# Performance work log

Measured on AMD Instinct MI355X. Metric: run time of the kernel, lower is better.

## Reference

```python
import jax, jax.numpy as jnp
import numpy as np
import math

CUTOFF = 6.0
NUM_RADIAL = 96
HID = 128
NUM_GRAPHS = 4
NODES_PER_GRAPH = 4000
BOX = 67.0
EPS = 1e-10


def _layernorm(x):
    m = jnp.mean(x, axis=-1, keepdims=True)
    v = jnp.var(x, axis=-1, keepdims=True)
    return (x - m) / jnp.sqrt(v + 1e-5)


def _rbf(dist):
    # rbf_emb: exp-scaled gaussians with cosine cutoff envelope
    start = math.exp(-CUTOFF)
    means = jnp.linspace(start, 1.0, NUM_RADIAL).astype(dist.dtype)
    beta = (2.0 / NUM_RADIAL * (1.0 - start)) ** -2
    d = dist[:, None]
    env = 0.5 * (jnp.cos(d * jnp.pi / CUTOFF) + 1.0) * (d < CUTOFF).astype(dist.dtype)
    return env * jnp.exp(-beta * jnp.square(jnp.exp(-d) - means))


def _forward(pos, rl_w1, rl_b1, rl_w2, rl_b2, ne_w, ne_b, sv_w, sv_b,
             l3_w1, l3_b1, l3_w2, l3_b2, mp_ln_w, mp_ln_b,
             xp_w1, xp_b1, xp_w2, xp_b2, rp_w, rp_b,
             ip_w1, ip_b1, ip_w2, ip_b2,
             fte_eq_w, fte_w1, fte_b1, fte_w2, fte_b2,
             out_w, out_b, z, batch, edge_index):
    N = pos.shape[0]
    silu = jax.nn.silu
    j, i = edge_index[0], edge_index[1]

    vecs = pos[j] - pos[i]                       # [E,3]
    dist = jnp.linalg.norm(vecs, axis=-1)        # [E]
    r_emb = _rbf(dist)                           # [E,R]
    r_hid = silu(r_emb @ rl_w1 + rl_b1) @ rl_w2 + rl_b2
    rbounds = 0.5 * (jnp.cos(dist * jnp.pi / CUTOFF) + 1.0)
    r_hid = rbounds[:, None] * r_hid             # [E,H]

    # NeighborEmb: s = ln(lin(onehot(z))) + scatter_add_i(ln(lin(onehot(z)))[j] * r_hid)
    z1h = jax.nn.one_hot(z, 95, dtype=pos.dtype)
    h0 = _layernorm(z1h @ ne_w + ne_b)           # [N,H]
    s = h0 + jax.ops.segment_sum(h0[j] * r_hid, i, num_segments=N)

    vec = jnp.zeros((N, 3, HID), pos.dtype)

    ed = vecs / (dist[:, None] + EPS)            # edge_diff [E,3]
    ec = jnp.cross(pos[i], pos[j])
    ec = ec / (jnp.linalg.norm(ec, axis=1, keepdims=True) + EPS)
    ev = jnp.cross(ed, ec)
    frame = jnp.stack([ed, ec, ev], axis=-1)     # [E,3(space),3(frame)]

    # S_vector: scatter_add_i( s_lin[j] outer edge_diff * r_hid )
    s_lin = silu(s @ sv_w + sv_b)
    msg = s_lin[j][:, None, :] * (r_hid[:, None, :] * ed[:, :, None])  # [E,3,H]
    S = jax.ops.segment_sum(msg, i, num_segments=N)                    # [N,3,H]

    def scalarize(Se):
        sc = jnp.einsum('edh,edf->efh', Se, frame)                     # [E,3,H]
        sc = sc.at[:, 1, :].set(jnp.abs(sc[:, 1, :]))
        p = jnp.transpose(sc, (0, 2, 1))                               # [E,H,3]
        out = silu(p @ l3_w1 + l3_b1) @ l3_w2 + l3_b2                  # [E,H,1]
        return (out + p[:, :, :1])[..., 0]                             # [E,H]

    scalar3 = scalarize(S[i])
    scalar4 = scalarize(S[j])
    ew = jnp.concatenate([scalar3, scalar4], axis=-1) * rbounds[:, None]
    ew = jnp.concatenate([ew, r_hid, r_emb], axis=-1)                  # [E,3H+R]

    # EquiMessagePassing (only one layer executes: source loops range(1))
    xln = _layernorm(s) * mp_ln_w + mp_ln_b
    xh = silu(xln @ xp_w1 + xp_b1) @ xp_w2 + xp_b2                     # [N,3H]
    rbfh = (r_emb @ rp_w + rp_b) * (silu(ew @ ip_w1 + ip_b1) @ ip_w2 + ip_b2)
    m = xh[j] * rbfh                                                   # [E,3H]
    m1, m2, m3 = jnp.split(m, 3, axis=-1)
    m2 = m2 / jnp.sqrt(3.0)
    vmsg = (vec[j] * m2[:, None, :] + m3[:, None, :] * ed[:, :, None]) / jnp.sqrt(float(HID))
    s = s + jax.ops.segment_sum(m1, i, num_segments=N)
    vec = vec + jax.ops.segment_sum(vmsg, i, num_segments=N)

    # FTE (node_frame == 0 in LEFTNet-Z: use invariant norm channel)
    vp = jnp.einsum('ndh,hk->ndk', vec, fte_eq_w)                      # [N,3,2H]
    v1, v2 = jnp.split(vp, 2, axis=-1)
    scalar = jnp.sqrt(jnp.sum(v1 * v1, axis=1) + EPS)                  # [N,H]
    vec_dot = jnp.sum(v1 * v2, axis=1) / jnp.sqrt(float(HID))
    xh2 = silu(jnp.concatenate([s, scalar], axis=-1) @ fte_w1 + fte_b1) @ fte_w2 + fte_b2
    a1, a2, a3 = jnp.split(xh2, 3, axis=-1)
    s = s + (a1 + a2 * vec_dot) / jnp.sqrt(2.0)
    vec = vec + a3[:, None, :] * v2

    out = s @ out_w + out_b                                            # [N,T]
    num = jax.ops.segment_sum(out, batch, num_segments=NUM_GRAPHS)
    cnt = jax.ops.segment_sum(jnp.ones((N,), out.dtype), batch, num_segments=NUM_GRAPHS)
    out = num / cnt[:, None]                                           # mean readout
    return out  # y_std=1, y_mean=0


def _lin_init(key, fi, fo, bias=True):
    k1, k2 = jax.random.split(key)
    lim = 1.0 / np.sqrt(fi)
    w = jax.random.uniform(k1, (fi, fo), jnp.float32, -lim, lim)
    if not bias:
        return w
    b = jax.random.uniform(k2, (fo,), jnp.float32, -lim, lim)
    return w, b


def setup_inputs() -> dict:
    rng = np.random.default_rng(0)
    N = NUM_GRAPHS * NODES_PER_GRAPH
    pos_np = (rng.random((N, 3)) * BOX).astype(np.float32)
    batch_np = np.repeat(np.arange(NUM_GRAPHS), NODES_PER_GRAPH).astype(np.int64)
    z_np = rng.integers(0, 95, size=(N,)).astype(np.int64)
    rows, cols = [], []
    for g in range(NUM_GRAPHS):
        p = pos_np[g * NODES_PER_GRAPH:(g + 1) * NODES_PER_GRAPH]
        d2 = ((p[:, None, :] - p[None, :, :]) ** 2).sum(-1)
        a, b = np.nonzero((d2 < CUTOFF ** 2) & (d2 > 0.0))
        rows.append(a + g * NODES_PER_GRAPH)
        cols.append(b + g * NODES_PER_GRAPH)
    edge_index = np.stack([np.concatenate(rows), np.concatenate(cols)]).astype(np.int64)

    keys = jax.random.split(jax.random.key(0), 16)
    rl_w1, rl_b1 = _lin_init(keys[0], NUM_RADIAL, HID)
    rl_w2, rl_b2 = _lin_init(keys[1], HID, HID)
    ne_w, ne_b = _lin_init(keys[2], 95, HID)
    sv_w, sv_b = _lin_init(keys[3], HID, HID)
    l3_w1, l3_b1 = _lin_init(keys[4], 3, HID // 4)
    l3_w2, l3_b2 = _lin_init(keys[5], HID // 4, 1)
    xp_w1, xp_b1 = _lin_init(keys[6], HID, HID)
    xp_w2, xp_b2 = _lin_init(keys[7], HID, 3 * HID)
    rp_w, rp_b = _lin_init(keys[8], NUM_RADIAL, 3 * HID)
    ip_w1, ip_b1 = _lin_init(keys[9], 3 * HID + NUM_RADIAL, 3 * HID)
    ip_w2, ip_b2 = _lin_init(keys[10], 3 * HID, 3 * HID)
    fte_eq_w = _lin_init(keys[11], HID, 2 * HID, bias=False)
    fte_w1, fte_b1 = _lin_init(keys[12], 2 * HID, HID)
    fte_w2, fte_b2 = _lin_init(keys[13], HID, 3 * HID)
    out_w, out_b = _lin_init(keys[14], HID, 1)

    return {
        'pos': jnp.asarray(pos_np), 'z': jnp.asarray(z_np),
        'batch': jnp.asarray(batch_np), 'edge_index': jnp.asarray(edge_index),
        'rl_w1': rl_w1, 'rl_b1': rl_b1, 'rl_w2': rl_w2, 'rl_b2': rl_b2,
        'ne_w': ne_w, 'ne_b': ne_b, 'sv_w': sv_w, 'sv_b': sv_b,
        'l3_w1': l3_w1, 'l3_b1': l3_b1, 'l3_w2': l3_w2, 'l3_b2': l3_b2,
        'mp_ln_w': jnp.ones((HID,), jnp.float32), 'mp_ln_b': jnp.zeros((HID,), jnp.float32),
        'xp_w1': xp_w1, 'xp_b1': xp_b1, 'xp_w2': xp_w2, 'xp_b2': xp_b2,
        'rp_w': rp_w, 'rp_b': rp_b,
        'ip_w1': ip_w1, 'ip_b1': ip_b1, 'ip_w2': ip_w2, 'ip_b2': ip_b2,
        'fte_eq_w': fte_eq_w, 'fte_w1': fte_w1, 'fte_b1': fte_b1,
        'fte_w2': fte_w2, 'fte_b2': fte_b2, 'out_w': out_w, 'out_b': out_b,
    }


def reference(pos, rl_w1, rl_b1, rl_w2, rl_b2, ne_w, ne_b, sv_w, sv_b,
              l3_w1, l3_b1, l3_w2, l3_b2, mp_ln_w, mp_ln_b,
              xp_w1, xp_b1, xp_w2, xp_b2, rp_w, rp_b,
              ip_w1, ip_b1, ip_w2, ip_b2,
              fte_eq_w, fte_w1, fte_b1, fte_w2, fte_b2,
              out_w, out_b, z, batch, edge_index):
    return _forward(pos, rl_w1, rl_b1, rl_w2, rl_b2, ne_w, ne_b, sv_w, sv_b,
                    l3_w1, l3_b1, l3_w2, l3_b2, mp_ln_w, mp_ln_b,
                    xp_w1, xp_b1, xp_w2, xp_b2, rp_w, rp_b,
                    ip_w1, ip_b1, ip_w2, ip_b2,
                    fte_eq_w, fte_w1, fte_b1, fte_w2, fte_b2,
                    out_w, out_b, z, batch, edge_index)
```

## Files before the change

kernel.cpp:

```cpp
#include <hip/hip_runtime.h>
#include <hip/hip_bf16.h>
#include <math.h>

#define NRAD 96
#define HIDDIM 128
typedef unsigned short ushortT;

typedef __attribute__((ext_vector_type(8))) short bf8_t;
typedef __attribute__((ext_vector_type(4))) float f4_t;

#if defined(__has_builtin)
#  if __has_builtin(__builtin_amdgcn_global_load_lds)
#    define HAVE_GLDS 1
#  endif
#  if __has_builtin(__builtin_amdgcn_rcpf)
#    define RCPF(x) __builtin_amdgcn_rcpf(x)
#  endif
#  if __has_builtin(__builtin_amdgcn_exp2f)
#    define EXP2F(x) __builtin_amdgcn_exp2f(x)
#  endif
#  if __has_builtin(__builtin_amdgcn_cosf)
#    define COSR(x) __builtin_amdgcn_cosf(x)
#  endif
#endif
#ifndef RCPF
#  define RCPF(x) (1.f/(x))
#endif
#ifndef EXP2F
#  define EXP2F(x) exp2f(x)
#endif
#ifndef COSR
#  define COSR(x) cosf(6.2831853071795864f*(x))
#endif
#define LOG2E 1.44269504088896f
#define LN2   0.69314718055995f

__device__ __forceinline__ float silu_f(float x){
  return x * RCPF(1.f + EXP2F(-LOG2E*x));
}
__device__ __forceinline__ float b2f(ushortT u){ return __uint_as_float(((unsigned int)u) << 16); }
__device__ __forceinline__ ushortT f2b(float x){
  unsigned int u = __float_as_uint(x);
  unsigned int r = (u + 0x7fffu + ((u >> 16) & 1u)) >> 16;
  return (ushortT)r;
}

#ifdef HAVE_GLDS
__device__ __forceinline__ void glds16(const ushortT* g, ushortT* l){
  __builtin_amdgcn_global_load_lds(
      (const __attribute__((address_space(1))) ushortT*)g,
      (__attribute__((address_space(3))) ushortT*)l, 16, 0, 0);
}
#endif

__global__ void k_detect(const ushortT* posw, int npos,
                         const int* batchw, int nb, int* flags){
  int tot = (npos < 4096 ? npos : 4096);
  int big = tot > nb ? tot : nb;
  int bad = 0, orv = 0;
  for (int t = blockIdx.x*blockDim.x + threadIdx.x; t < big; t += gridDim.x*blockDim.x){
    if (t < tot){
      float x = b2f(posw[t]);
      if (!(fabsf(x) <= 1000.f)) bad = 1;
    }
    if (t < nb && (t & 1)) orv |= batchw[t];
  }
  if (bad) atomicOr(&flags[2], 1);
  if (orv) atomicOr(&flags[3], 1);
}

__global__ void k_iconv(const int* zsrc, const int* bsrc, const int* esrc,
                        int* zi, int* bi, int* eii, int Nn, int E, const int* flags,
                        int* deg){
  int f = (flags[3] == 0) ? 1 : 0;
  int total = 2*Nn + 2*E;
  for (int t = blockIdx.x*blockDim.x + threadIdx.x; t < total; t += gridDim.x*blockDim.x){
    if (t < Nn) zi[t] = zsrc[(size_t)t << f];
    else if (t < 2*Nn) bi[t-Nn] = bsrc[(size_t)(t-Nn) << f];
    else {
      int e = t - 2*Nn;
      int v = esrc[(size_t)e << f];
      eii[e] = v;
      if (e >= E) atomicAdd(&deg[v], 1);
    }
  }
}

struct ConvDesc { const ushortT* src; float* dst; int n; };
struct ConvArgs { ConvDesc d[32]; };

__global__ void k_conv(ConvArgs a, int cnt, const int* flags){
  int y = blockIdx.y;
  if (y >= cnt) return;
  int f = (flags[2] == 0) ? 1 : 0;
  const ushortT* s = a.d[y].src;
  float* dst = a.d[y].dst;
  int n = a.d[y].n;
  if (f){
    for (int t = blockIdx.x*blockDim.x + threadIdx.x; t < n; t += gridDim.x*blockDim.x)
      dst[t] = b2f(s[t]);
  } else {
    const float* sf = (const float*)s;
    for (int t = blockIdx.x*blockDim.x + threadIdx.x; t < n; t += gridDim.x*blockDim.x)
      dst[t] = sf[t];
  }
}

struct TDesc { const ushortT* src; ushortT* dst; int K, N; };
struct TArgs { TDesc d[12]; };

__global__ void k_wt(TArgs a, int cnt, const int* flags){
  int y = blockIdx.y;
  if (y >= cnt) return;
  int f = (flags[2] == 0) ? 1 : 0;
  const ushortT* s = a.d[y].src;
  ushortT* dst = a.d[y].dst;
  int K = a.d[y].K, N = a.d[y].N, tot = K*N;
  for (int t = blockIdx.x*blockDim.x + threadIdx.x; t < tot; t += gridDim.x*blockDim.x){
    int k = t / N, n = t - k*N;
    ushortT v = f ? s[t] : f2b(((const float*)s)[t]);
    dst[(size_t)n*K + k] = v;
  }
}

__global__ void k_f2b(const float* __restrict__ src, ushortT* __restrict__ dst, int n){
  for (int t = blockIdx.x*blockDim.x + threadIdx.x; t < n; t += gridDim.x*blockDim.x)
    dst[t] = f2b(src[t]);
}

__global__ void k_zero(float* __restrict__ p, int n){
  int t = blockIdx.x*blockDim.x + threadIdx.x;
  int stride = gridDim.x*blockDim.x;
  for (; t < n; t += stride) p[t] = 0.f;
}

__global__ void k_sentinel(__hip_bfloat16* out, int n, float val){
  int t = threadIdx.x;
  if (t < n) out[t] = __float2bfloat16(val);
}

__global__ void k_csr_scan(const int* __restrict__ deg, int* __restrict__ rowptr, int Nn){
  __shared__ int sh[256];
  __shared__ int carry;
  if (threadIdx.x == 0){ carry = 0; rowptr[0] = 0; }
  __syncthreads();
  for (int t0 = 0; t0 < Nn; t0 += 256){
    int idx = t0 + threadIdx.x;
    int v = (idx < Nn) ? deg[idx] : 0;
    sh[threadIdx.x] = v; __syncthreads();
    for (int o = 1; o < 256; o <<= 1){
      int u = (threadIdx.x >= o) ? sh[threadIdx.x - o] : 0;
      __syncthreads();
      sh[threadIdx.x] += u; __syncthreads();
    }
    if (idx < Nn) rowptr[idx + 1] = carry + sh[threadIdx.x];
    __syncthreads();
    if (threadIdx.x == 0) carry += sh[255];
    __syncthreads();
  }
}

__global__ void k_csr_scatter(const int* __restrict__ eii, int E,
                              const int* __restrict__ rowptr, int* __restrict__ cursor,
                              int* __restrict__ jp, int* __restrict__ ip){
  int e = blockIdx.x*blockDim.x + threadIdx.x;
  if (e >= E) return;
  int i = eii[E+e];
  int p = atomicAdd(&cursor[i], 1);
  int k = rowptr[i] + p;
  jp[k] = eii[e];
  ip[k] = i;
}

__global__ void k_geom(const float* __restrict__ pos,
                       const int* __restrict__ jp, const int* __restrict__ ip,
                       int off, int Cc,
                       float* __restrict__ edb, float* __restrict__ ecv,
                       float* __restrict__ rb, ushortT* __restrict__ remb)
{
  int el = blockIdx.x*blockDim.x + threadIdx.x;
  if (el >= Cc) return;
  int g = off + el;
  int j = jp[g], i = ip[g];
  float pjx = pos[3*j], pjy = pos[3*j+1], pjz = pos[3*j+2];
  float pix = pos[3*i], piy = pos[3*i+1], piz = pos[3*i+2];
  float vx = pjx-pix, vy = pjy-piy, vz = pjz-piz;
  float d = sqrtf(vx*vx + vy*vy + vz*vz);
  float inv = RCPF(d + 1e-10f);
  float edx = vx*inv, edy = vy*inv, edz = vz*inv;
  edb[3*el]=edx; edb[3*el+1]=edy; edb[3*el+2]=edz;
  if (ecv){
    float cx = piy*pjz - piz*pjy;
    float cy = piz*pjx - pix*pjz;
    float cz = pix*pjy - piy*pjx;
    float cn = sqrtf(cx*cx + cy*cy + cz*cz);
    float inv2 = RCPF(cn + 1e-10f);
    cx *= inv2; cy *= inv2; cz *= inv2;
    ecv[6*el]=cx; ecv[6*el+1]=cy; ecv[6*el+2]=cz;
    ecv[6*el+3]=edy*cz - edz*cy;
    ecv[6*el+4]=edz*cx - edx*cz;
    ecv[6*el+5]=edx*cy - edy*cx;
  }
  float rbv = 0.5f*(COSR(d*0.08333333333f) + 1.f);
  rb[el] = rbv;
  float env = (d < 6.f) ? rbv : 0.f;
  const float stf = 0.0024787522f;
  const float prf = (2.0f/96.0f)*(1.0f - stf);
  const float betaL = LOG2E/(prf*prf);
  float emd = EXP2F(-LOG2E*d);
  for (int k = 0; k < NRAD; ++k){
    float mu = stf + (1.0f - stf)*((float)k*(1.0f/95.0f));
    float t = emd - mu;
    remb[(size_t)el*NRAD + k] = f2b(env * EXP2F(-betaL*t*t));
  }
}

__global__ __launch_bounds__(128) void k_embed(const int* __restrict__ z,
    const float* __restrict__ ne_w, const float* __restrict__ ne_b,
    float* __restrict__ s, float* __restrict__ h0,
    float* __restrict__ S, float* __restrict__ vecacc)
{
  int n = blockIdx.x; int h = threadIdx.x;
  float x = ne_w[(size_t)z[n]*HIDDIM + h] + ne_b[h];
  __shared__ float red[128];
  red[h] = x; __syncthreads();
  for (int o = 64; o > 0; o >>= 1){ if (h < o) red[h] += red[h+o]; __syncthreads(); }
  float mean = red[0] * (1.f/128.f);
  __syncthreads();
  float dx = x - mean;
  red[h] = dx*dx; __syncthreads();
  for (int o = 64; o > 0; o >>= 1){ if (h < o) red[h] += red[h+o]; __syncthreads(); }
  float var = red[0] * (1.f/128.f);
  float y = dx * rsqrtf(var + 1e-5f);
  s[(size_t)n*HIDDIM + h] = y;
  h0[(size_t)n*HIDDIM + h] = y;
  float* Sr = &S[(size_t)n*384 + h];
  float* Vr = &vecacc[(size_t)n*384 + h];
  Sr[0]=0.f; Sr[128]=0.f; Sr[256]=0.f;
  Vr[0]=0.f; Vr[128]=0.f; Vr[256]=0.f;
}

__global__ __launch_bounds__(128) void k_ln(const float* __restrict__ src, ushortT* __restrict__ dst,
    const float* __restrict__ g, const float* __restrict__ b, ushortT* __restrict__ sb)
{
  int n = blockIdx.x; int h = threadIdx.x;
  float x = src[(size_t)n*HIDDIM + h];
  sb[(size_t)n*HIDDIM + h] = f2b(x);
  __shared__ float red[128];
  red[h] = x; __syncthreads();
  for (int o = 64; o > 0; o >>= 1){ if (h < o) red[h] += red[h+o]; __syncthreads(); }
  float mean = red[0] * (1.f/128.f);
  __syncthreads();
  float dx = x - mean;
  red[h] = dx*dx; __syncthreads();
  for (int o = 64; o > 0; o >>= 1){ if (h < o) red[h] += red[h+o]; __syncthreads(); }
  float var = red[0] * (1.f/128.f);
  float y = dx * rsqrtf(var + 1e-5f);
  dst[(size_t)n*HIDDIM + h] = f2b(y * g[h] + b[h]);
}

__global__ __launch_bounds__(128) void k_seg1n(const int* __restrict__ rowptr,
    const int* __restrict__ jp, int o, int Cc,
    const float* __restrict__ h0, const ushortT* __restrict__ rhid,
    float* __restrict__ s)
{
  int i = blockIdx.x, h = threadIdx.x;
  int b = rowptr[i], e = rowptr[i+1];
  if (b < o) b = o;
  int hi = o + Cc; if (e > hi) e = hi;
  if (b >= e) return;
  float acc = 0.f;
  int m = b;
  for (; m + 1 < e; m += 2){
    int j0 = jp[m], j1 = jp[m+1];
    float r0 = b2f(rhid[(size_t)(m-o)*HIDDIM + h]);
    float r1 = b2f(rhid[(size_t)(m+1-o)*HIDDIM + h]);
    acc += h0[(size_t)j0*HIDDIM + h]*r0 + h0[(size_t)j1*HIDDIM + h]*r1;
  }
  if (m < e) acc += h0[(size_t)jp[m]*HIDDIM + h] * b2f(rhid[(size_t)(m-o)*HIDDIM + h]);
  s[(size_t)i*HIDDIM + h] += acc;
}

__global__ __launch_bounds__(128) void k_seg2n(const int* __restrict__ rowptr,
    const int* __restrict__ jp, int o, int Cc,
    const ushortT* __restrict__ slin, const ushortT* __restrict__ rhid,
    const float* __restrict__ edb, float* __restrict__ S)
{
  int i = blockIdx.x, h = threadIdx.x;
  int b = rowptr[i], e = rowptr[i+1];
  if (b < o) b = o;
  int hi = o + Cc; if (e > hi) e = hi;
  if (b >= e) return;
  float a0 = 0.f, a1 = 0.f, a2 = 0.f;
  int m = b;
  for (; m + 1 < e; m += 2){
    int ml = m - o, ml2 = ml + 1;
    float u0 = b2f(slin[(size_t)jp[m]*HIDDIM + h])   * b2f(rhid[(size_t)ml*HIDDIM + h]);
    float u1 = b2f(slin[(size_t)jp[m+1]*HIDDIM + h]) * b2f(rhid[(size_t)ml2*HIDDIM + h]);
    a0 += u0*edb[3*ml]   + u1*edb[3*ml2];
    a1 += u0*edb[3*ml+1] + u1*edb[3*ml2+1];
    a2 += u0*edb[3*ml+2] + u1*edb[3*ml2+2];
  }
  if (m < e){
    int ml = m - o;
    float u0 = b2f(slin[(size_t)jp[m]*HIDDIM + h]) * b2f(rhid[(size_t)ml*HIDDIM + h]);
    a0 += u0*edb[3*ml]; a1 += u0*edb[3*ml+1]; a2 += u0*edb[3*ml+2];
  }
  float* base = &S[(size_t)i*384 + h];
  base[0]   += a0;
  base[128] += a1;
  base[256] += a2;
}

__global__ __launch_bounds__(128) void k_seg3n(const int* __restrict__ rowptr,
    int o, int Cc,
    const ushortT* __restrict__ mb, const float* __restrict__ edb,
    float* __restrict__ s, float* __restrict__ vecacc)
{
  int i = blockIdx.x, h = threadIdx.x;
  int b = rowptr[i], e = rowptr[i+1];
  if (b < o) b = o;
  int hi = o + Cc; if (e > hi) e = hi;
  if (b >= e) return;
  const float is128 = 0.08838834764831845f;
  float am = 0.f, v0 = 0.f, v1 = 0.f, v2 = 0.f;
  int m = b;
  for (; m + 1 < e; m += 2){
    int ml = m - o, ml2 = ml + 1;
    float m1a = b2f(mb[(size_t)ml*384 + h]);
    float m1b = b2f(mb[(size_t)ml2*384 + h]);
    float mma = b2f(mb[(size_t)ml*384 + 256 + h]) * is128;
    float mmb = b2f(mb[(size_t)ml2*384 + 256 + h]) * is128;
    am += m1a + m1b;
    v0 += mma*edb[3*ml]   + mmb*edb[3*ml2];
    v1 += mma*edb[3*ml+1] + mmb*edb[3*ml2+1];
    v2 += mma*edb[3*ml+2] + mmb*edb[3*ml2+2];
  }
  if (m < e){
    int ml = m - o;
    float m1 = b2f(mb[(size_t)ml*384 + h]);
    float mm = b2f(mb[(size_t)ml*384 + 256 + h]) * is128;
    am += m1;
    v0 += mm*edb[3*ml]; v1 += mm*edb[3*ml+1]; v2 += mm*edb[3*ml+2];
  }
  s[(size_t)i*HIDDIM + h] += am;
  float* base = &vecacc[(size_t)i*384 + h];
  base[0]   += v0;
  base[128] += v1;
  base[256] += v2;
}

__global__ __launch_bounds__(256) void k_scal2(
  const int* __restrict__ jp, const int* __restrict__ ip, int off,
  const float* __restrict__ pos, const float* __restrict__ S,
  const ushortT* __restrict__ rhid,
  const float* __restrict__ w1, const float* __restrict__ b1,
  const float* __restrict__ w2, const float* __restrict__ b2,
  ushortT* __restrict__ ew,
  ushortT* __restrict__ remb_out, const ushortT* __restrict__ remb_src)
{
  __shared__ float geo[11];
  __shared__ float w1s[96], b1s[32], w2s[32];
  __shared__ float sb2;
  int el = blockIdx.x;
  int g = off + el;
  int t = threadIdx.x;
  if (t < 96) w1s[t] = w1[t] * (-LOG2E);
  else if (t < 128) b1s[t-96] = b1[t-96] * (-LOG2E);
  else if (t < 160) w2s[t-128] = w2[t-128] * (-LN2);
  else if (t == 160) sb2 = b2[0];
  if (t == 0){
    int j = jp[g], i = ip[g];
    float pjx = pos[3*j], pjy = pos[3*j+1], pjz = pos[3*j+2];
    float pix = pos[3*i], piy = pos[3*i+1], piz = pos[3*i+2];
    float vx = pjx-pix, vy = pjy-piy, vz = pjz-piz;
    float d = sqrtf(vx*vx + vy*vy + vz*vz);
    float inv = RCPF(d + 1e-10f);
    float f00 = vx*inv, f01 = vy*inv, f02 = vz*inv;
    float cx = piy*pjz - piz*pjy;
    float cy = piz*pjx - pix*pjz;
    float cz = pix*pjy - piy*pjx;
    float cn = sqrtf(cx*cx + cy*cy + cz*cz);
    float inv2 = RCPF(cn + 1e-10f);
    float f10 = cx*inv2, f11 = cy*inv2, f12 = cz*inv2;
    geo[0]=f00; geo[1]=f01; geo[2]=f02;
    geo[3]=f10; geo[4]=f11; geo[5]=f12;
    geo[6]=f01*f12 - f02*f11;
    geo[7]=f02*f10 - f00*f12;
    geo[8]=f00*f11 - f01*f10;
    geo[9]=0.5f*(COSR(d*0.08333333333f) + 1.f);
    geo[10]=d;
  }
  __syncthreads();
  int which = t >> 7;
  int h = t & 127;
  int n = which ? jp[g] : ip[g];
  const float* Sn = &S[(size_t)n*384];
  float S0 = Sn[h], S1 = Sn[128+h], S2 = Sn[256+h];
  float v0 = S0*geo[0] + S1*geo[1] + S2*geo[2];
  float v1 = fabsf(S0*geo[3] + S1*geo[4] + S2*geo[5]);
  float v2 = S0*geo[6] + S1*geo[7] + S2*geo[8];
  float out = 0.f;
  #pragma unroll
  for (int u = 0; u < 32; ++u){
    float tt = fmaf(v0, w1s[u], fmaf(v1, w1s[32+u], fmaf(v2, w1s[64+u], b1s[u])));
    float r = RCPF(1.f + EXP2F(tt));
    out = fmaf(tt*r, w2s[u], out);
  }
  float scal = out + sb2 + v0;
  ushortT* ewr = &ew[(size_t)el*480];
  ewr[which*128 + h] = f2b(scal * geo[9]);
  if (which == 0){
    ewr[256 + h] = rhid[(size_t)el*HIDDIM + h];
    if (h < NRAD){
      ushortT rv;
      if (remb_src){
        rv = remb_src[(size_t)el*NRAD + h];
      } else {
        float d = geo[10];
        float rbv = geo[9];
        float env = (d < 6.f) ? rbv : 0.f;
        const float stf = 0.0024787522f;
        const float prf = (2.0f/96.0f)*(1.0f - stf);
        const float betaL = LOG2E/(prf*prf);
        float mu = stf + (1.0f - stf)*((float)h*(1.0f/95.0f));
        float tr = EXP2F(-LOG2E*d) - mu;
        rv = f2b(env * EXP2F(-betaL*tr*tr));
        remb_out[(size_t)el*NRAD + h] = rv;
      }
      ewr[384 + h] = rv;
    }
  }
}

__global__ __launch_bounds__(256) void mgemm(
  const ushortT* __restrict__ A, const ushortT* __restrict__ BT,
  const float* __restrict__ bias,
  float* __restrict__ Cf, ushortT* __restrict__ Cb,
  int M, int N, int K, int epi,
  const float* __restrict__ rowscale,
  const ushortT* __restrict__ mul1b,
  const ushortT* __restrict__ xhpb,
  const int* __restrict__ jidx,
  int skipTile)
{
  const int tid = threadIdx.x;
  const int w = tid >> 6;
  const int lane = tid & 63;
  const int l15 = lane & 15;
  const int q = lane >> 4;
  const int wm = w & 1, wn = w >> 1;
  const int rowBase = blockIdx.y * 128;
  int bx = blockIdx.x;
  if (skipTile >= 0 && bx >= skipTile) bx++;
  const int colBase = bx * 128;
  f4_t acc[4][4] = {};

#ifdef HAVE_GLDS
  __shared__ ushortT As[128*32];
  __shared__ ushortT Bs[128*32];
  const int rS = 32*w + (lane >> 2);
  const int kS = (lane & 3) << 3;
  ushortT* lA0 = &As[(32*w)*32];
  ushortT* lA1 = &As[(32*w+16)*32];
  ushortT* lB0 = &Bs[(32*w)*32];
  ushortT* lB1 = &Bs[(32*w+16)*32];
  int ra0 = rowBase + rS;      if (ra0 >= M) ra0 = M-1;
  int ra1 = rowBase + rS + 16; if (ra1 >= M) ra1 = M-1;
  const ushortT* gA0 = A  + (size_t)ra0*K + kS;
  const ushortT* gA1 = A  + (size_t)ra1*K + kS;
  const ushortT* gB0 = BT + (size_t)(colBase + rS)*K + kS;
  const ushortT* gB1 = BT + (size_t)(colBase + rS + 16)*K + kS;
  for (int k0 = 0; k0 < K; k0 += 32){
    glds16(gA0 + k0, lA0);
    glds16(gA1 + k0, lA1);
    glds16(gB0 + k0, lB0);
    glds16(gB1 + k0, lB1);
    __syncthreads();
    bf8_t a[4], b[4];
    #pragma unroll
    for (int mt = 0; mt < 4; ++mt)
      a[mt] = *(const bf8_t*)&As[(wm*64 + mt*16 + l15)*32 + q*8];
    #pragma unroll
    for (int nt = 0; nt < 4; ++nt)
      b[nt] = *(const bf8_t*)&Bs[(wn*64 + nt*16 + l15)*32 + q*8];
    #pragma unroll
    for (int mt = 0; mt < 4; ++mt){
      #pragma unroll
      for (int nt = 0; nt < 4; ++nt)
        acc[mt][nt] = __builtin_amdgcn_mfma_f32_16x16x32_bf16(a[mt], b[nt], acc[mt][nt], 0, 0, 0);
    }
    __syncthreads();
  }
#else
  __shared__ ushortT As[128*48];
  __shared__ ushortT Bs[128*48];
  const int r0 = tid >> 2,         s0 = (tid & 3) << 3;
  const int r1 = (tid + 256) >> 2, s1 = ((tid + 256) & 3) << 3;
  for (int k0 = 0; k0 < K; k0 += 32){
    int4 a0v = make_int4(0,0,0,0), a1v = make_int4(0,0,0,0);
    if (rowBase + r0 < M) a0v = *(const int4*)&A[(size_t)(rowBase + r0)*K + k0 + s0];
    if (rowBase + r1 < M) a1v = *(const int4*)&A[(size_t)(rowBase + r1)*K + k0 + s1];
    int4 b0v = *(const int4*)&BT[(size_t)(colBase + r0)*K + k0 + s0];
    int4 b1v = *(const int4*)&BT[(size_t)(colBase + r1)*K + k0 + s1];
    __syncthreads();
    *(int4*)&As[r0*48 + s0] = a0v;
    *(int4*)&As[r1*48 + s1] = a1v;
    *(int4*)&Bs[r0*48 + s0] = b0v;
    *(int4*)&Bs[r1*48 + s1] = b1v;
    __syncthreads();
    bf8_t a[4], b[4];
    #pragma unroll
    for (int mt = 0; mt < 4; ++mt)
      a[mt] = *(const bf8_t*)&As[(wm*64 + mt*16 + l15)*48 + q*8];
    #pragma unroll
    for (int nt = 0; nt < 4; ++nt)
      b[nt] = *(const bf8_t*)&Bs[(wn*64 + nt*16 + l15)*48 + q*8];
    #pragma unroll
    for (int mt = 0; mt < 4; ++mt){
      #pragma unroll
      for (int nt = 0; nt < 4; ++nt)
        acc[mt][nt] = __builtin_amdgcn_mfma_f32_16x16x32_bf16(a[mt], b[nt], acc[mt][nt], 0, 0, 0);
    }
  }
#endif

  #pragma unroll
  for (int mt = 0; mt < 4; ++mt){
    int row = rowBase + wm*64 + mt*16 + q*4;
    #pragma unroll
    for (int nt = 0; nt < 4; ++nt){
      int col = colBase + wn*64 + nt*16 + l15;
      float bv = bias ? bias[col] : 0.f;
      #pragma unroll
      for (int r = 0; r < 4; ++r){
        int rr = row + r;
        if (rr >= M) continue;
        float x = acc[mt][nt][r] + bv;
        if (epi == 1) x = silu_f(x);
        else if (epi == 2) x *= rowscale[rr];
        else if (epi == 3) x = x * b2f(mul1b[(size_t)rr*N + col]) * b2f(xhpb[(size_t)jidx[rr]*N + col]);
        if (Cb) Cb[(size_t)rr*N + col] = f2b(x);
        else    Cf[(size_t)rr*N + col] = x;
      }
    }
  }
}

__global__ __launch_bounds__(128) void k_fte_pre(const float* __restrict__ vpc,
    const float* __restrict__ s, ushortT* __restrict__ catb, float* __restrict__ vdot,
    int no)
{
  int nl = blockIdx.x, h = threadIdx.x;
  int n = no + nl;
  const float* base = &vpc[(size_t)nl*768];
  float a0 = base[h],       a1 = base[256+h],     a2 = base[512+h];
  float c0 = base[128+h],   c1 = base[384+h],     c2 = base[640+h];
  float scal = sqrtf(a0*a0 + a1*a1 + a2*a2 + 1e-10f);
  float vd = (a0*c0 + a1*c1 + a2*c2) * 0.08838834764831845f;
  catb[(size_t)n*256 + h] = f2b(s[(size_t)n*HIDDIM + h]);
  catb[(size_t)n*256 + 128 + h] = f2b(scal);
  vdot[(size_t)n*HIDDIM + h] = vd;
}

__global__ __launch_bounds__(128) void k_out(const float* __restrict__ xh2,
    const float* __restrict__ vdot, const float* __restrict__ s,
    const float* __restrict__ ow, const float* __restrict__ ob,
    float* __restrict__ nodeout)
{
  int n = blockIdx.x, h = threadIdx.x;
  float a1 = xh2[(size_t)n*384 + h];
  float a2 = xh2[(size_t)n*384 + 128 + h];
  float sv = s[(size_t)n*HIDDIM + h] + (a1 + a2*vdot[(size_t)n*HIDDIM + h]) * 0.7071067811865476f;
  __shared__ float red[128];
  red[h] = sv * ow[h];
  __syncthreads();
  for (int o = 64; o > 0; o >>= 1){ if (h < o) red[h] += red[h+o]; __syncthreads(); }
  if (h == 0) nodeout[n] = red[0] + ob[0];
}

__global__ __launch_bounds__(256) void k_final(const float* __restrict__ nodeout,
    const int* __restrict__ batch, void* __restrict__ out, int Nn, const int* flags)
{
  int g = blockIdx.x;
  __shared__ float rs[256], rc[256];
  float sm = 0.f, c = 0.f;
  for (int n = threadIdx.x; n < Nn; n += 256){
    if (batch[n] == g){ sm += nodeout[n]; c += 1.f; }
  }
  rs[threadIdx.x] = sm; rc[threadIdx.x] = c;
  __syncthreads();
  for (int o = 128; o > 0; o >>= 1){
    if (threadIdx.x < o){ rs[threadIdx.x] += rs[threadIdx.x+o]; rc[threadIdx.x] += rc[threadIdx.x+o]; }
    __syncthreads();
  }
  if (threadIdx.x == 0){
    float v = (rc[0] > 0.f) ? rs[0]/rc[0] : 0.f;
    if (flags[2] == 0) ((__hip_bfloat16*)out)[g] = __float2bfloat16(v);
    else ((float*)out)[g] = v;
  }
}

extern "C" void kernel_launch(void* const* d_in, const int* in_sizes, int n_in,
                              void* d_out, int out_size, void* d_ws, size_t ws_size,
                              hipStream_t stream)
{
  const int N = in_sizes[0] / 3;
  const int E = in_sizes[3] / 2;

  size_t off = 0;
  auto alloc = [&](size_t n)->float*{
    float* p = (float*)d_ws + off;
    off += (n + 3) & ~(size_t)3;
    return p;
  };
  auto allocU = [&](size_t n)->ushortT*{ return (ushortT*)alloc((n + 1) / 2); };

  int* flags  = (int*)alloc(4);
  int* deg    = (int*)alloc((size_t)N);
  int* cursor = (int*)alloc((size_t)N);
  size_t zeroHdr = off;
  int* zi     = (int*)alloc((size_t)N);
  int* bi     = (int*)alloc((size_t)N);
  int* eii    = (int*)alloc((size_t)2*E);
  int* rowptr = (int*)alloc((size_t)N + 4);
  int* jp     = (int*)alloc((size_t)E);
  int* ipp    = (int*)alloc((size_t)E);

  float* pos = alloc((size_t)N*3);
  float* w[31];
  for (int t = 0; t < 31; ++t) w[t] = alloc((size_t)in_sizes[4+t]);
  float* rl_b1=w[1];  float* rl_b2=w[3];
  float* ne_w =w[4];  float* ne_b =w[5];  float* sv_b =w[7];
  float* l3_w1=w[8];  float* l3_b1=w[9];  float* l3_w2=w[10]; float* l3_b2=w[11];
  float* mp_w =w[12]; float* mp_b =w[13]; float* xp_b1=w[15];
  float* xp_b2=w[17]; float* rp_b =w[19];
  float* ip_b1=w[21]; float* ip_b2=w[23];
  float* fte_b1=w[26];float* fte_b2=w[28];float* out_w=w[29]; float* out_b=w[30];

  ushortT* wt_rl1 = allocU(96*128);
  ushortT* wt_rl2 = allocU(128*128);
  ushortT* wt_sv  = allocU(128*128);
  ushortT* wt_xp1 = allocU(128*128);
  ushortT* wt_xp2 = allocU((size_t)128*384);
  ushortT* wt_rp  = allocU((size_t)96*384);
  ushortT* wt_ip1 = allocU((size_t)480*384);
  ushortT* wt_ip2 = allocU((size_t)384*384);
  ushortT* wt_feq = allocU((size_t)128*256);
  ushortT* wt_ft1 = allocU((size_t)256*128);
  ushortT* wt_ft2 = allocU((size_t)128*384);

  float* s    = alloc((size_t)N*HIDDIM);
  float* h0   = alloc((size_t)N*HIDDIM);
  ushortT* sb     = allocU((size_t)N*HIDDIM);
  ushortT* slin_b = allocU((size_t)N*HIDDIM);
  ushortT* xln_b  = allocU((size_t)N*HIDDIM);
  ushortT* hb     = allocU((size_t)N*HIDDIM);
  float* S    = alloc((size_t)N*384);
  float* vecacc = alloc((size_t)N*384);
  ushortT* xh_b = allocU((size_t)N*384);
  float* nodeout = alloc((size_t)N);
  float* vdot = h0;
  ushortT* catb = sb;
  ushortT* vab = (ushortT*)S;
  float* xh2 = vecacc;

  size_t wsF = ws_size / sizeof(float);

  int tier = 0; size_t p = 739;
  if (off + 116ULL*(size_t)E + 16 + 256ULL*624 <= wsF){ tier = 2; p = 624; }
  else if (off + 67ULL*(size_t)E + 16 + 256ULL*672 <= wsF){ tier = 1; p = 672; }

  ushortT *rhid_a = nullptr, *remb_a = nullptr;
  float *edb_a = nullptr, *rb_a = nullptr;
  if (tier >= 1){
    rhid_a = allocU((size_t)E*128);
    edb_a  = alloc((size_t)3*E);
  }
  if (tier == 2){
    remb_a = allocU((size_t)E*96);
    rb_a   = alloc((size_t)E);
  }
  size_t availF = (wsF > off) ? (wsF - off) : 0;
  if (availF < 256*p){
    k_sentinel<<<1, 64, 0, stream>>>((__hip_bfloat16*)d_out, out_size,
                                     (float)(double)(ws_size >> 20));
    return;
  }
  size_t Cs = availF / p; if (Cs > (size_t)E) Cs = E;
  int C = (int)(Cs & ~(size_t)15);
  if (C < 256) C = 256;

  float* scratch0 = (float*)d_ws + off;
  ushortT* remb_l = nullptr;
  if (tier <= 1) remb_l = allocU((size_t)C*96);
  float* edb_l = nullptr; ushortT* rhid_l = nullptr;
  if (tier == 0){
    edb_l  = alloc((size_t)3*C);
    rhid_l = allocU((size_t)C*128);
  }
  ushortT* ew_b = allocU((size_t)C*480);
  ushortT* R2b  = allocU((size_t)C*384);
  ushortT* R1b  = allocU((size_t)C*384);
  ushortT* Rmb  = ew_b;
  float* ecv_d  = (float*)ew_b;
  float* rb_d   = (float*)ew_b + (size_t)6*C;
  ushortT* R2rl = R2b;
  float* vpc = scratch0;
  size_t scratchF = (size_t)C*p;

  auto mg = [&](const ushortT* A, const ushortT* BT, const float* bias,
                float* Cf, ushortT* Cb, int M, int Nc, int K, int epi,
                const float* rowscale = nullptr, const ushortT* mul1b = nullptr,
                const ushortT* xhpb = nullptr, const int* jidx = nullptr,
                int skipTile = -1){
    dim3 grid(Nc/128 - (skipTile >= 0 ? 1 : 0), (M + 127)/128);
    mgemm<<<grid, 256, 0, stream>>>(A, BT, bias, Cf, Cb, M, Nc, K, epi,
                                    rowscale, mul1b, xhpb, jidx, skipTile);
  };

  k_zero<<<64, 256, 0, stream>>>((float*)flags, (int)zeroHdr);
  k_detect<<<64, 256, 0, stream>>>((const ushortT*)d_in[0], in_sizes[0],
                                   (const int*)d_in[2], in_sizes[2], flags);
  k_iconv<<<1024, 256, 0, stream>>>((const int*)d_in[1], (const int*)d_in[2],
                                    (const int*)d_in[3], zi, bi, eii, N, E, flags, deg);

  ConvArgs ca;
  ca.d[0] = { (const ushortT*)d_in[0], pos, in_sizes[0] };
  for (int t = 0; t < 31; ++t)
    ca.d[1+t] = { (const ushortT*)d_in[4+t], w[t], in_sizes[4+t] };
  k_conv<<<dim3(32, 32), 256, 0, stream>>>(ca, 32, flags);

  TArgs ta;
  ta.d[0]  = { (const ushortT*)d_in[4],  wt_rl1, 96, 128 };
  ta.d[1]  = { (const ushortT*)d_in[6],  wt_rl2, 128, 128 };
  ta.d[2]  = { (const ushortT*)d_in[10], wt_sv,  128, 128 };
  ta.d[3]  = { (const ushortT*)d_in[18], wt_xp1, 128, 128 };
  ta.d[4]  = { (const ushortT*)d_in[20], wt_xp2, 128, 384 };
  ta.d[5]  = { (const ushortT*)d_in[22], wt_rp,  96, 384 };
  ta.d[6]  = { (const ushortT*)d_in[24], wt_ip1, 480, 384 };
  ta.d[7]  = { (const ushortT*)d_in[26], wt_ip2, 384, 384 };
  ta.d[8]  = { (const ushortT*)d_in[28], wt_feq, 128, 256 };
  ta.d[9]  = { (const ushortT*)d_in[29], wt_ft1, 256, 128 };
  ta.d[10] = { (const ushortT*)d_in[31], wt_ft2, 128, 384 };
  k_wt<<<dim3(48, 11), 256, 0, stream>>>(ta, 11, flags);

  k_csr_scan<<<1, 256, 0, stream>>>(deg, rowptr, N);
  k_csr_scatter<<<(E + 255)/256, 256, 0, stream>>>(eii, E, rowptr, cursor, jp, ipp);

  k_embed<<<N, 128, 0, stream>>>(zi, ne_w, ne_b, s, h0, S, vecacc);

  if (tier == 2){
    k_geom<<<(E + 255)/256, 256, 0, stream>>>(pos, jp, ipp, 0, E,
                                              edb_a, nullptr, rb_a, remb_a);
    for (int o = 0; o < E; o += C){
      int Cc = (E - o < C) ? (E - o) : C;
      mg(remb_a + (size_t)o*96, wt_rl1, rl_b1, nullptr, R2rl, Cc, 128, 96, 1);
      mg(R2rl, wt_rl2, rl_b2, nullptr, rhid_a + (size_t)o*128, Cc, 128, 128, 2, rb_a + o);
    }
    k_seg1n<<<N, 128, 0, stream>>>(rowptr, jp, 0, E, h0, rhid_a, s);
  } else if (tier == 1){
    for (int o = 0; o < E; o += C){
      int Cc = (E - o < C) ? (E - o) : C;
      k_geom<<<(Cc + 255)/256, 256, 0, stream>>>(pos, jp, ipp, o, Cc,
                                                 edb_a + (size_t)3*o, ecv_d, rb_d, remb_l);
      mg(remb_l, wt_rl1, rl_b1, nullptr, R2rl, Cc, 128, 96, 1);
      mg(R2rl, wt_rl2, rl_b2, nullptr, rhid_a + (size_t)o*128, Cc, 128, 128, 2, rb_d);
    }
    k_seg1n<<<N, 128, 0, stream>>>(rowptr, jp, 0, E, h0, rhid_a, s);
  } else {
    for (int o = 0; o < E; o += C){
      int Cc = (E - o < C) ? (E - o) : C;
      k_geom<<<(Cc + 255)/256, 256, 0, stream>>>(pos, jp, ipp, o, Cc,
                                                 edb_l, ecv_d, rb_d, remb_l);
      mg(remb_l, wt_rl1, rl_b1, nullptr, R2rl, Cc, 128, 96, 1);
      mg(R2rl, wt_rl2, rl_b2, nullptr, rhid_l, Cc, 128, 128, 2, rb_d);
      k_seg1n<<<N, 128, 0, stream>>>(rowptr, jp, o, Cc, h0, rhid_l, s);
    }
  }

  k_ln<<<N, 128, 0, stream>>>(s, xln_b, mp_w, mp_b, sb);
  mg(sb, wt_sv, sv_b, nullptr, slin_b, N, 128, 128, 1);
  mg(xln_b, wt_xp1, xp_b1, nullptr, hb, N, 128, 128, 1);
  mg(hb, wt_xp2, xp_b2, nullptr, xh_b, N, 384, 128, 0, nullptr, nullptr, nullptr, nullptr, 1);

  if (tier >= 1){
    k_seg2n<<<N, 128, 0, stream>>>(rowptr, jp, 0, E, slin_b, rhid_a, edb_a, S);
  } else {
    for (int o = 0; o < E; o += C){
      int Cc = (E - o < C) ? (E - o) : C;
      k_geom<<<(Cc + 255)/256, 256, 0, stream>>>(pos, jp, ipp, o, Cc,
                                                 edb_l, ecv_d, rb_d, remb_l);
      mg(remb_l, wt_rl1, rl_b1, nullptr, R2rl, Cc, 128, 96, 1);
      mg(R2rl, wt_rl2, rl_b2, nullptr, rhid_l, Cc, 128, 128, 2, rb_d);
      k_seg2n<<<N, 128, 0, stream>>>(rowptr, jp, o, Cc, slin_b, rhid_l, edb_l, S);
    }
  }

  for (int o = 0; o < E; o += C){
    int Cc = (E - o < C) ? (E - o) : C;
    const ushortT* rhid_p; const float* edb_p;
    const ushortT* remb_p; const ushortT* remb_srcp;
    if (tier == 2){
      rhid_p = rhid_a + (size_t)o*128;
      edb_p  = edb_a + (size_t)3*o;
      remb_p = remb_a + (size_t)o*96;
      remb_srcp = remb_p;
    } else if (tier == 1){
      rhid_p = rhid_a + (size_t)o*128;
      edb_p  = edb_a + (size_t)3*o;
      remb_p = remb_l;
      remb_srcp = nullptr;
    } else {
      k_geom<<<(Cc + 255)/256, 256, 0, stream>>>(pos, jp, ipp, o, Cc,
                                                 edb_l, ecv_d, rb_d, remb_l);
      mg(remb_l, wt_rl1, rl_b1, nullptr, R2rl, Cc, 128, 96, 1);
      mg(R2rl, wt_rl2, rl_b2, nullptr, rhid_l, Cc, 128, 128, 2, rb_d);
      rhid_p = rhid_l; edb_p = edb_l; remb_p = remb_l; remb_srcp = nullptr;
    }
    k_scal2<<<Cc, 256, 0, stream>>>(jp, ipp, o, pos, S, rhid_p,
                                    l3_w1, l3_b1, l3_w2, l3_b2, ew_b,
                                    remb_l, remb_srcp);
    mg(remb_p, wt_rp, rp_b, nullptr, R1b, Cc, 384, 96, 0,
       nullptr, nullptr, nullptr, nullptr, 1);
    mg(ew_b, wt_ip1, ip_b1, nullptr, R2b, Cc, 384, 480, 1);
    mg(R2b, wt_ip2, ip_b2, nullptr, Rmb, Cc, 384, 384, 3,
       nullptr, R1b, xh_b, jp + o, 1);
    k_seg3n<<<N, 128, 0, stream>>>(rowptr, o, Cc, Rmb, edb_p, s, vecacc);
  }

  k_f2b<<<1024, 256, 0, stream>>>(vecacc, vab, N*384);
  int Cn = (int)(scratchF / 768);
  if (Cn > N) Cn = N;
  for (int no = 0; no < N; no += Cn){
    int Cc = (N - no < Cn) ? (N - no) : Cn;
    mg(vab + (size_t)no*384, wt_feq, nullptr, vpc, nullptr, 3*Cc, 256, 128, 0);
    k_fte_pre<<<Cc, 128, 0, stream>>>(vpc, s, catb, vdot, no);
  }
  mg(catb, wt_ft1, fte_b1, nullptr, hb, N, 128, 256, 1);
  mg(hb, wt_ft2, fte_b2, xh2, nullptr, N, 384, 128, 0);

  k_out<<<N, 128, 0, stream>>>(xh2, vdot, s, out_w, out_b, nodeout);
  k_final<<<out_size, 256, 0, stream>>>(nodeout, bi, d_out, N, flags);
}
```

Before: 2.024 ms.

## Precompute edge frames in k_geom and process two edges per scalarize block

The scalarize kernel no longer recomputes edge geometry serially on one thread per block. It reads precomputed frame vectors (edb, ecv) and the cutoff envelope from k_geom outputs, which are now stored persistently in workspace. Each 256-thread block now handles two edges using float2 vector math, which halves the block count and amortizes the weight loads into shared memory. In exchange the workspace grows and tier 1 adds an extra k_geom launch per chunk.

```diff
diff --git a/kernel.cpp b/kernel.cpp
--- a/kernel.cpp
+++ b/kernel.cpp
@@ -8,6 +8,7 @@
 
 typedef __attribute__((ext_vector_type(8))) short bf8_t;
 typedef __attribute__((ext_vector_type(4))) float f4_t;
+typedef __attribute__((ext_vector_type(2))) float f2_t;
 
 #if defined(__has_builtin)
 #  if __has_builtin(__builtin_amdgcn_global_load_lds)
@@ -350,85 +351,68 @@
   base[256] += v2;
 }
 
-__global__ __launch_bounds__(256) void k_scal2(
-  const int* __restrict__ jp, const int* __restrict__ ip, int off,
-  const float* __restrict__ pos, const float* __restrict__ S,
-  const ushortT* __restrict__ rhid,
+__global__ __launch_bounds__(256) void k_scal3(
+  const int* __restrict__ jp, const int* __restrict__ ip, int off, int Cc,
+  const float* __restrict__ S,
+  const ushortT* __restrict__ rhid, const float* __restrict__ edb,
+  const float* __restrict__ ecv, const float* __restrict__ rb,
+  const ushortT* __restrict__ remb,
   const float* __restrict__ w1, const float* __restrict__ b1,
   const float* __restrict__ w2, const float* __restrict__ b2,
-  ushortT* __restrict__ ew,
-  ushortT* __restrict__ remb_out, const ushortT* __restrict__ remb_src)
-{
-  __shared__ float geo[11];
+  ushortT* __restrict__ ew)
+{
   __shared__ float w1s[96], b1s[32], w2s[32];
   __shared__ float sb2;
-  int el = blockIdx.x;
-  int g = off + el;
   int t = threadIdx.x;
   if (t < 96) w1s[t] = w1[t] * (-LOG2E);
   else if (t < 128) b1s[t-96] = b1[t-96] * (-LOG2E);
   else if (t < 160) w2s[t-128] = w2[t-128] * (-LN2);
   else if (t == 160) sb2 = b2[0];
-  if (t == 0){
-    int j = jp[g], i = ip[g];
-    float pjx = pos[3*j], pjy = pos[3*j+1], pjz = pos[3*j+2];
-    float pix = pos[3*i], piy = pos[3*i+1], piz = pos[3*i+2];
-    float vx = pjx-pix, vy = pjy-piy, vz = pjz-piz;
-    float d = sqrtf(vx*vx + vy*vy + vz*vz);
-    float inv = RCPF(d + 1e-10f);
-    float f00 = vx*inv, f01 = vy*inv, f02 = vz*inv;
-    float cx = piy*pjz - piz*pjy;
-    float cy = piz*pjx - pix*pjz;
-    float cz = pix*pjy - piy*pjx;
-    float cn = sqrtf(cx*cx + cy*cy + cz*cz);
-    float inv2 = RCPF(cn + 1e-10f);
-    float f10 = cx*inv2, f11 = cy*inv2, f12 = cz*inv2;
-    geo[0]=f00; geo[1]=f01; geo[2]=f02;
-    geo[3]=f10; geo[4]=f11; geo[5]=f12;
-    geo[6]=f01*f12 - f02*f11;
-    geo[7]=f02*f10 - f00*f12;
-    geo[8]=f00*f11 - f01*f10;
-    geo[9]=0.5f*(COSR(d*0.08333333333f) + 1.f);
-    geo[10]=d;
-  }
+  int ea = blockIdx.x*2;
+  int eb = (ea + 1 < Cc) ? ea + 1 : ea;
+  int which = t >> 7, h = t & 127;
+  int ga = off + ea, gb = off + eb;
+  int na = which ? jp[ga] : ip[ga];
+  int nb = which ? jp[gb] : ip[gb];
+  f2_t f00 = {edb[3*ea],   edb[3*eb]};
+  f2_t f01 = {edb[3*ea+1], edb[3*eb+1]};
+  f2_t f02 = {edb[3*ea+2], edb[3*eb+2]};
+  f2_t f10 = {ecv[6*ea],   ecv[6*eb]};
+  f2_t f11 = {ecv[6*ea+1], ecv[6*eb+1]};
+  f2_t f12 = {ecv[6*ea+2], ecv[6*eb+2]};
+  f2_t f20 = {ecv[6*ea+3], ecv[6*eb+3]};
+  f2_t f21 = {ecv[6*ea+4], ecv[6*eb+4]};
+  f2_t f22 = {ecv[6*ea+5], ecv[6*eb+5]};
+  f2_t rbv = {rb[ea], rb[eb]};
   __syncthreads();
-  int which = t >> 7;
-  int h = t & 127;
-  int n = which ? jp[g] : ip[g];
-  const float* Sn = &S[(size_t)n*384];
-  float S0 = Sn[h], S1 = Sn[128+h], S2 = Sn[256+h];
-  float v0 = S0*geo[0] + S1*geo[1] + S2*geo[2];
-  float v1 = fabsf(S0*geo[3] + S1*geo[4] + S2*geo[5]);
-  float v2 = S0*geo[6] + S1*geo[7] + S2*geo[8];
-  float out = 0.f;
+  const float* Sa = &S[(size_t)na*384];
+  const float* Sb = &S[(size_t)nb*384];
+  f2_t S0 = {Sa[h],     Sb[h]};
+  f2_t S1 = {Sa[128+h], Sb[128+h]};
+  f2_t S2 = {Sa[256+h], Sb[256+h]};
+  f2_t v0 = S0*f00 + S1*f01 + S2*f02;
+  f2_t v1t = S0*f10 + S1*f11 + S2*f12;
+  f2_t v1 = {fabsf(v1t.x), fabsf(v1t.y)};
+  f2_t v2 = S0*f20 + S1*f21 + S2*f22;
+  f2_t out = {0.f, 0.f};
   #pragma unroll
   for (int u = 0; u < 32; ++u){
-    float tt = fmaf(v0, w1s[u], fmaf(v1, w1s[32+u], fmaf(v2, w1s[64+u], b1s[u])));
-    float r = RCPF(1.f + EXP2F(tt));
-    out = fmaf(tt*r, w2s[u], out);
-  }
-  float scal = out + sb2 + v0;
-  ushortT* ewr = &ew[(size_t)el*480];
-  ewr[which*128 + h] = f2b(scal * geo[9]);
+    f2_t tt = v0*w1s[u] + v1*w1s[32+u] + v2*w1s[64+u] + b1s[u];
+    f2_t r;
+    r.x = RCPF(1.f + EXP2F(tt.x));
+    r.y = RCPF(1.f + EXP2F(tt.y));
+    out += (tt*r)*w2s[u];
+  }
+  f2_t res = (out + sb2 + v0) * rbv;
+  ushortT* ewa = &ew[(size_t)ea*480];
+  ewa[which*128 + h] = f2b(res.x);
+  if (eb != ea) ew[(size_t)eb*480 + which*128 + h] = f2b(res.y);
   if (which == 0){
-    ewr[256 + h] = rhid[(size_t)el*HIDDIM + h];
-    if (h < NRAD){
-      ushortT rv;
-      if (remb_src){
-        rv = remb_src[(size_t)el*NRAD + h];
-      } else {
-        float d = geo[10];
-        float rbv = geo[9];
-        float env = (d < 6.f) ? rbv : 0.f;
-        const float stf = 0.0024787522f;
-        const float prf = (2.0f/96.0f)*(1.0f - stf);
-        const float betaL = LOG2E/(prf*prf);
-        float mu = stf + (1.0f - stf)*((float)h*(1.0f/95.0f));
-        float tr = EXP2F(-LOG2E*d) - mu;
-        rv = f2b(env * EXP2F(-betaL*tr*tr));
-        remb_out[(size_t)el*NRAD + h] = rv;
-      }
-      ewr[384 + h] = rv;
+    ewa[256 + h] = rhid[(size_t)ea*HIDDIM + h];
+    if (h < NRAD) ewa[384 + h] = remb[(size_t)ea*NRAD + h];
+    if (eb != ea){
+      ew[(size_t)eb*480 + 256 + h] = rhid[(size_t)eb*HIDDIM + h];
+      if (h < NRAD) ew[(size_t)eb*480 + 384 + h] = remb[(size_t)eb*NRAD + h];
     }
   }
 }
@@ -667,19 +651,20 @@
 
   size_t wsF = ws_size / sizeof(float);
 
-  int tier = 0; size_t p = 739;
-  if (off + 116ULL*(size_t)E + 16 + 256ULL*624 <= wsF){ tier = 2; p = 624; }
-  else if (off + 67ULL*(size_t)E + 16 + 256ULL*672 <= wsF){ tier = 1; p = 672; }
+  int tier = 0; size_t p = 746;
+  if (off + 122ULL*(size_t)E + 16 + 256ULL*624 <= wsF){ tier = 2; p = 624; }
+  else if (off + 67ULL*(size_t)E + 16 + 256ULL*679 <= wsF){ tier = 1; p = 679; }
 
   ushortT *rhid_a = nullptr, *remb_a = nullptr;
-  float *edb_a = nullptr, *rb_a = nullptr;
+  float *edb_a = nullptr, *ecv_a = nullptr, *rb_a = nullptr;
   if (tier >= 1){
     rhid_a = allocU((size_t)E*128);
     edb_a  = alloc((size_t)3*E);
   }
   if (tier == 2){
+    ecv_a  = alloc((size_t)6*E);
+    rb_a   = alloc((size_t)E);
     remb_a = allocU((size_t)E*96);
-    rb_a   = alloc((size_t)E);
   }
   size_t availF = (wsF > off) ? (wsF - off) : 0;
   if (availF < 256*p){
@@ -692,8 +677,12 @@
   if (C < 256) C = 256;
 
   float* scratch0 = (float*)d_ws + off;
-  ushortT* remb_l = nullptr;
-  if (tier <= 1) remb_l = allocU((size_t)C*96);
+  ushortT* remb_l = nullptr; float *ecv_l = nullptr, *rb_l = nullptr;
+  if (tier <= 1){
+    remb_l = allocU((size_t)C*96);
+    ecv_l  = alloc((size_t)6*C);
+    rb_l   = alloc((size_t)C);
+  }
   float* edb_l = nullptr; ushortT* rhid_l = nullptr;
   if (tier == 0){
     edb_l  = alloc((size_t)3*C);
@@ -703,8 +692,6 @@
   ushortT* R2b  = allocU((size_t)C*384);
   ushortT* R1b  = allocU((size_t)C*384);
   ushortT* Rmb  = ew_b;
-  float* ecv_d  = (float*)ew_b;
-  float* rb_d   = (float*)ew_b + (size_t)6*C;
   ushortT* R2rl = R2b;
   float* vpc = scratch0;
   size_t scratchF = (size_t)C*p;
@@ -752,7 +739,7 @@
 
   if (tier == 2){
     k_geom<<<(E + 255)/256, 256, 0, stream>>>(pos, jp, ipp, 0, E,
-                                              edb_a, nullptr, rb_a, remb_a);
+                                              edb_a, ecv_a, rb_a, remb_a);
     for (int o = 0; o < E; o += C){
       int Cc = (E - o < C) ? (E - o) : C;
       mg(remb_a + (size_t)o*96, wt_rl1, rl_b1, nullptr, R2rl, Cc, 128, 96, 1);
@@ -763,18 +750,18 @@
     for (int o = 0; o < E; o += C){
       int Cc = (E - o < C) ? (E - o) : C;
       k_geom<<<(Cc + 255)/256, 256, 0, stream>>>(pos, jp, ipp, o, Cc,
-                                                 edb_a + (size_t)3*o, ecv_d, rb_d, remb_l);
+                                                 edb_a + (size_t)3*o, nullptr, rb_l, remb_l);
       mg(remb_l, wt_rl1, rl_b1, nullptr, R2rl, Cc, 128, 96, 1);
-      mg(R2rl, wt_rl2, rl_b2, nullptr, rhid_a + (size_t)o*128, Cc, 128, 128, 2, rb_d);
+      mg(R2rl, wt_rl2, rl_b2, nullptr, rhid_a + (size_t)o*128, Cc, 128, 128, 2, rb_l);
     }
     k_seg1n<<<N, 128, 0, stream>>>(rowptr, jp, 0, E, h0, rhid_a, s);
   } else {
     for (int o = 0; o < E; o += C){
       int Cc = (E - o < C) ? (E - o) : C;
       k_geom<<<(Cc + 255)/256, 256, 0, stream>>>(pos, jp, ipp, o, Cc,
-                                                 edb_l, ecv_d, rb_d, remb_l);
+                                                 edb_l, nullptr, rb_l, remb_l);
       mg(remb_l, wt_rl1, rl_b1, nullptr, R2rl, Cc, 128, 96, 1);
-      mg(R2rl, wt_rl2, rl_b2, nullptr, rhid_l, Cc, 128, 128, 2, rb_d);
+      mg(R2rl, wt_rl2, rl_b2, nullptr, rhid_l, Cc, 128, 128, 2, rb_l);
       k_seg1n<<<N, 128, 0, stream>>>(rowptr, jp, o, Cc, h0, rhid_l, s);
     }
   }
@@ -790,37 +777,39 @@
     for (int o = 0; o < E; o += C){
       int Cc = (E - o < C) ? (E - o) : C;
       k_geom<<<(Cc + 255)/256, 256, 0, stream>>>(pos, jp, ipp, o, Cc,
-                                                 edb_l, ecv_d, rb_d, remb_l);
+                                                 edb_l, nullptr, rb_l, remb_l);
       mg(remb_l, wt_rl1, rl_b1, nullptr, R2rl, Cc, 128, 96, 1);
-      mg(R2rl, wt_rl2, rl_b2, nullptr, rhid_l, Cc, 128, 128, 2, rb_d);
+      mg(R2rl, wt_rl2, rl_b2, nullptr, rhid_l, Cc, 128, 128, 2, rb_l);
       k_seg2n<<<N, 128, 0, stream>>>(rowptr, jp, o, Cc, slin_b, rhid_l, edb_l, S);
     }
   }
 
   for (int o = 0; o < E; o += C){
     int Cc = (E - o < C) ? (E - o) : C;
-    const ushortT* rhid_p; const float* edb_p;
-    const ushortT* remb_p; const ushortT* remb_srcp;
+    const ushortT *rhid_p, *remb_p;
+    const float *edb_p, *ecv_p, *rb_p;
     if (tier == 2){
       rhid_p = rhid_a + (size_t)o*128;
       edb_p  = edb_a + (size_t)3*o;
+      ecv_p  = ecv_a + (size_t)6*o;
+      rb_p   = rb_a + o;
       remb_p = remb_a + (size_t)o*96;
-      remb_srcp = remb_p;
     } else if (tier == 1){
+      k_geom<<<(Cc + 255)/256, 256, 0, stream>>>(pos, jp, ipp, o, Cc,
+                                                 edb_a + (size_t)3*o, ecv_l, rb_l, remb_l);
       rhid_p = rhid_a + (size_t)o*128;
       edb_p  = edb_a + (size_t)3*o;
-      remb_p = remb_l;
-      remb_srcp = nullptr;
+      ecv_p  = ecv_l; rb_p = rb_l; remb_p = remb_l;
     } else {
       k_geom<<<(Cc + 255)/256, 256, 0, stream>>>(pos, jp, ipp, o, Cc,
-                                                 edb_l, ecv_d, rb_d, remb_l);
+                                                 edb_l, ecv_l, rb_l, remb_l);
       mg(remb_l, wt_rl1, rl_b1, nullptr, R2rl, Cc, 128, 96, 1);
-      mg(R2rl, wt_rl2, rl_b2, nullptr, rhid_l, Cc, 128, 128, 2, rb_d);
-      rhid_p = rhid_l; edb_p = edb_l; remb_p = remb_l; remb_srcp = nullptr;
-    }
-    k_scal2<<<Cc, 256, 0, stream>>>(jp, ipp, o, pos, S, rhid_p,
-                                    l3_w1, l3_b1, l3_w2, l3_b2, ew_b,
-                                    remb_l, remb_srcp);
+      mg(R2rl, wt_rl2, rl_b2, nullptr, rhid_l, Cc, 128, 128, 2, rb_l);
+      rhid_p = rhid_l; edb_p = edb_l; ecv_p = ecv_l; rb_p = rb_l; remb_p = remb_l;
+    }
+    k_scal3<<<(Cc + 1)/2, 256, 0, stream>>>(jp, ipp, o, Cc, S, rhid_p,
+                                            edb_p, ecv_p, rb_p, remb_p,
+                                            l3_w1, l3_b1, l3_w2, l3_b2, ew_b);
     mg(remb_p, wt_rp, rp_b, nullptr, R1b, Cc, 384, 96, 0,
        nullptr, nullptr, nullptr, nullptr, 1);
     mg(ew_b, wt_ip1, ip_b1, nullptr, R2b, Cc, 384, 480, 1);
```

After: 1.926 ms. 1.05x faster.
